# Kernel optimization log

Hardware: AMD Instinct MI355X
Metric: run time of the kernel (lower is better)

Reference implementation:

```python
import jax, jax.numpy as jnp
import numpy as np

HEADS = 8
DIM_HEAD = 64
ROPE_BASE = 10000.0


def _rope_rotate(t):
    """lucidrains-style interleaved RoPE on t: [B, H, N, D]."""
    n, d = t.shape[-2], t.shape[-1]
    inv_freq = 1.0 / (ROPE_BASE ** (jnp.arange(0, d, 2, dtype=jnp.float32) / d))  # [D/2]
    freqs = jnp.arange(n, dtype=jnp.float32)[:, None] * inv_freq[None, :]          # [N, D/2]
    freqs = jnp.repeat(freqs, 2, axis=-1)                                           # [N, D], interleaved
    cos = jnp.cos(freqs).astype(t.dtype)
    sin = jnp.sin(freqs).astype(t.dtype)
    # rotate_half with interleaved pairs: (x1, x2) -> (-x2, x1)
    t2 = t.reshape(t.shape[:-1] + (d // 2, 2))
    rot = jnp.stack([-t2[..., 1], t2[..., 0]], axis=-1).reshape(t.shape)
    return t * cos + rot * sin


def setup_inputs() -> dict:
    key = jax.random.key(0)
    k1, k2, k3, k4 = jax.random.split(key, 4)
    B, N, DIM = 8, 1024, 512
    hidden = HEADS * DIM_HEAD  # 512
    x = jax.random.normal(k1, (B, N, DIM), dtype=jnp.float32)
    pos_bias = jax.random.normal(k2, (HEADS, N, N), dtype=jnp.float32) * 0.1
    w_qkv = jax.random.normal(k3, (DIM, hidden * 3), dtype=jnp.float32) * (DIM ** -0.5)
    w_out = jax.random.normal(k4, (hidden, DIM), dtype=jnp.float32) * (hidden ** -0.5)
    return {"x": x, "pos_bias": pos_bias, "w_qkv": w_qkv, "w_out": w_out}


def reference(x, pos_bias, w_qkv, w_out):
    B, N, _ = x.shape
    qkv = x @ w_qkv                                   # [B, N, 3*H*D]
    q, k, v = jnp.split(qkv, 3, axis=-1)

    def split_heads(t):
        return t.reshape(B, N, HEADS, DIM_HEAD).transpose(0, 2, 1, 3)  # [B, H, N, D]

    q, k, v = map(split_heads, (q, k, v))
    q = q * (DIM_HEAD ** -0.5)
    q = _rope_rotate(q)
    k = _rope_rotate(k)
    sim = jnp.einsum('bhid,bhjd->bhij', q, k) + pos_bias  # pos_bias [H,N,N] broadcasts over B
    attn = jax.nn.softmax(sim, axis=-1)                    # max-subtracted softmax (stable)
    out = jnp.einsum('bhij,bhjd->bhid', attn, v)
    out = out.transpose(0, 2, 1, 3).reshape(B, N, HEADS * DIM_HEAD)
    return out @ w_out
```

## Files before the change

### kernel.cpp

```cpp
#include <hip/hip_runtime.h>

#define DEV __device__ __forceinline__

typedef __attribute__((ext_vector_type(8))) short bf16x8;
typedef __attribute__((ext_vector_type(4))) short bf16x4;
typedef __attribute__((ext_vector_type(4))) float f32x4;
typedef __attribute__((ext_vector_type(4))) unsigned int u32x4;

constexpr int Bb = 8;
constexpr int Nn = 1024;
constexpr int DIMm = 512;
constexpr int Hh = 8;
constexpr int Dh = 64;
constexpr int Mm = Bb * Nn;
constexpr float LN10K = 9.210340371976184f;
constexpr float LOG2E = 1.4426950408889634f;

DEV short f2bf(float f) {
  unsigned int u = __float_as_uint(f);
  u += 0x7fffu + ((u >> 16) & 1u);
  return (short)(u >> 16);
}

DEV unsigned int cvtpk(float lo, float hi) {
  unsigned int r;
  asm("v_cvt_pk_bf16_f32 %0, %1, %2" : "=v"(r) : "v"(lo), "v"(hi));
  return r;
}

DEV bf16x8 comb(bf16x4 lo, bf16x4 hi) {
  bf16x8 r;
  r[0] = lo[0]; r[1] = lo[1]; r[2] = lo[2]; r[3] = lo[3];
  r[4] = hi[0]; r[5] = hi[1]; r[6] = hi[2]; r[7] = hi[3];
  return r;
}

DEV f32x4 mfma16(bf16x8 a, bf16x8 b, f32x4 c) {
  return __builtin_amdgcn_mfma_f32_16x16x32_bf16(a, b, c, 0, 0, 0);
}

DEV void gload16(const void* g, void* l) {
  __builtin_amdgcn_global_load_lds(
      (const __attribute__((address_space(1))) void*)g,
      (__attribute__((address_space(3))) void*)l, 16, 0, 0);
}

__global__ void prep_kernel(const float* __restrict__ x, const float* __restrict__ wq,
                            const float* __restrict__ wo, short* __restrict__ x_bf,
                            short* __restrict__ wqkvT, short* __restrict__ woutT,
                            float2* __restrict__ tab) {
  int stride = gridDim.x * blockDim.x;
  int t = blockIdx.x * blockDim.x + threadIdx.x;
  for (int i = t; i < Mm * DIMm / 4; i += stride) {
    float4 v = ((const float4*)x)[i];
    bf16x4 o;
    o[0] = f2bf(v.x); o[1] = f2bf(v.y); o[2] = f2bf(v.z); o[3] = f2bf(v.w);
    *(bf16x4*)(x_bf + (size_t)i * 4) = o;
  }
  for (int i = t; i < 1536 * 512; i += stride) {
    int n = i >> 9, k = i & 511;
    wqkvT[i] = f2bf(wq[(size_t)k * 1536 + n]);
  }
  for (int i = t; i < 512 * 512; i += stride) {
    int n = i >> 9, k = i & 511;
    woutT[i] = f2bf(wo[(size_t)k * 512 + n]);
  }
  for (int i = t; i < Nn * 32; i += stride) {
    int n = i >> 5, d2 = i & 31;
    float fr = (float)n * __expf(-(float)(2 * d2) * (LN10K / 64.f));
    float sn, cs;
    __sincosf(fr, &sn, &cs);
    tab[i] = make_float2(cs, sn);
  }
}

template <int QKV>
__global__ __launch_bounds__(256) void gemm_k(const short* __restrict__ A,
                                              const short* __restrict__ Bt,
                                              float* __restrict__ outF,
                                              short* __restrict__ qr,
                                              short* __restrict__ kr,
                                              short* __restrict__ vt,
                                              const float2* __restrict__ tab) {
  __shared__ short Al[128][40];
  __shared__ short Bl[128][40];
  const int tid = threadIdx.x;
  const int lane = tid & 63;
  const int wid = tid >> 6;
  const int wm = wid >> 1, wn = wid & 1;
  const int li = lane & 15, g4 = (lane >> 4) << 2;
  const int m0 = blockIdx.x * 128, n0 = blockIdx.y * 128;

  f32x4 zero4 = {0.f, 0.f, 0.f, 0.f};
  f32x4 acc[4][4];
#pragma unroll
  for (int i = 0; i < 4; ++i)
#pragma unroll
    for (int j = 0; j < 4; ++j) acc[i][j] = zero4;

  for (int kt = 0; kt < 512; kt += 32) {
#pragma unroll
    for (int p = 0; p < 2; ++p) {
      int e = (tid + p * 256) * 8;
      int r = e >> 5, c = e & 31;
      *(u32x4*)(&Al[r][c]) = *(const u32x4*)(A + (size_t)(m0 + r) * 512 + kt + c);
      *(u32x4*)(&Bl[r][c]) = *(const u32x4*)(Bt + (size_t)(n0 + r) * 512 + kt + c);
    }
    __syncthreads();
    bf16x8 af[4], bfr[4];
#pragma unroll
    for (int mt = 0; mt < 4; ++mt) {
      int row = wm * 64 + mt * 16 + li;
      af[mt] = comb(*(const bf16x4*)(&Al[row][g4]), *(const bf16x4*)(&Al[row][16 + g4]));
    }
#pragma unroll
    for (int nt = 0; nt < 4; ++nt) {
      int row = wn * 64 + nt * 16 + li;
      bfr[nt] = comb(*(const bf16x4*)(&Bl[row][g4]), *(const bf16x4*)(&Bl[row][16 + g4]));
    }
#pragma unroll
    for (int mt = 0; mt < 4; ++mt)
#pragma unroll
      for (int nt = 0; nt < 4; ++nt)
        acc[mt][nt] = mfma16(af[mt], bfr[nt], acc[mt][nt]);
    __syncthreads();
  }

  if (QKV == 0) {
#pragma unroll
    for (int mt = 0; mt < 4; ++mt) {
      int mb = m0 + wm * 64 + mt * 16 + g4;
#pragma unroll
      for (int nt = 0; nt < 4; ++nt) {
        int c = n0 + wn * 64 + nt * 16 + li;
#pragma unroll
        for (int r = 0; r < 4; ++r) outF[(size_t)(mb + r) * 512 + c] = acc[mt][nt][r];
      }
    }
  } else {
    const int sec = n0 >> 9;
#pragma unroll
    for (int mt = 0; mt < 4; ++mt) {
      int mb = m0 + wm * 64 + mt * 16 + g4;
      int b_ = mb >> 10;
      int nb = mb & 1023;
#pragma unroll
      for (int nt = 0; nt < 4; ++nt) {
        int c = n0 + wn * 64 + nt * 16 + li;
        int cs = c & 511;
        int hh = cs >> 6, d = cs & 63;
        size_t bhoff = (size_t)(b_ * Hh + hh) * 65536;
        if (sec == 2) {
          int dt = d >> 4, liD = d & 15;
          int kkJ = (nb >> 5) & 1;
          int gj = (nb & 15) >> 2;
          int s0 = (nb & 16) >> 2;
          size_t off = bhoff + (size_t)(nb >> 6) * 4096 +
                       (size_t)((dt * 2 + kkJ) * 512) + (size_t)(liD + 16 * gj) * 8 + s0;
          uint2 st;
          st.x = cvtpk(acc[mt][nt][0], acc[mt][nt][1]);
          st.y = cvtpk(acc[mt][nt][2], acc[mt][nt][3]);
          *(uint2*)(vt + off) = st;
        } else {
          int kkD = d >> 5;
          int gd = (d & 15) >> 2;
          int sD = (d & 3) | ((d & 16) >> 2);
          size_t off = bhoff + (size_t)(nb >> 4) * 1024 + (size_t)(kkD * 512) +
                       (size_t)((nb & 15) + 16 * gd) * 8 + sD;
          short* dst = (sec == 0 ? qr : kr) + off;
#pragma unroll
          for (int r = 0; r < 4; ++r) {
            float v0 = acc[mt][nt][r];
            float vp = __shfl_xor(v0, 1, 64);
            float2 cssn = tab[(size_t)(nb + r) * 32 + (d >> 1)];
            float rot = (d & 1) ? vp : -vp;
            float res = v0 * cssn.x + rot * cssn.y;
            if (sec == 0) res *= 0.125f;
            dst[(size_t)r * 8] = f2bf(res);
          }
        }
      }
    }
  }
}

constexpr int KVB = 64;
constexpr int NTT = Nn / KVB;

__global__ __launch_bounds__(256, 4) void attn_k(const short* __restrict__ qf_g,
                                                 const short* __restrict__ kf_g,
                                                 const short* __restrict__ vf_g,
                                                 const float* __restrict__ bias,
                                                 short* __restrict__ ao) {
  __shared__ short Kls[2][4096];
  __shared__ short Vls[2][4096];
  const int tid = threadIdx.x, lane = tid & 63, w = tid >> 6;
  const int li = lane & 15, g4 = (lane >> 4) << 2;
  const int bid = blockIdx.x;
  const int h = bid & 7;
  const int b_ = (bid >> 3) & 7;
  const int it = bid >> 6;
  const int bh = b_ * 8 + h;
  const int i0 = it * 64;
  const int iq = i0 + w * 16 + li;

  const short* qbase = qf_g + (size_t)bh * 65536 + (size_t)(it * 4 + w) * 1024 + lane * 8;
  bf16x8 qf0 = *(const bf16x8*)(qbase);
  bf16x8 qf1 = *(const bf16x8*)(qbase + 512);

  const short* kb = kf_g + (size_t)bh * 65536;
  const short* vb = vf_g + (size_t)bh * 65536;
  const float* br = bias + ((size_t)h * Nn + iq) * Nn + g4;

  float m_run = -1e30f, l_run = 0.f;
  f32x4 zero4 = {0.f, 0.f, 0.f, 0.f};
  f32x4 acc[4];
#pragma unroll
  for (int i = 0; i < 4; ++i) acc[i] = zero4;

#define STAGE_TILE(T, BUF)                                                  \
  do {                                                                      \
    const short* ks_ = kb + (size_t)(T) * 4096;                             \
    const short* vs_ = vb + (size_t)(T) * 4096;                             \
    gload16(ks_ + (size_t)tid * 8, &Kls[BUF][(size_t)(w * 64) * 8]);        \
    gload16(ks_ + (size_t)(256 + tid) * 8,                                  \
            &Kls[BUF][(size_t)(256 + w * 64) * 8]);                         \
    gload16(vs_ + (size_t)tid * 8, &Vls[BUF][(size_t)(w * 64) * 8]);        \
    gload16(vs_ + (size_t)(256 + tid) * 8,                                  \
            &Vls[BUF][(size_t)(256 + w * 64) * 8]);                         \
  } while (0)

  f32x4 bbA[4], bbB[4];

  STAGE_TILE(0, 0);
#pragma unroll
  for (int js = 0; js < 4; ++js) bbA[js] = *(const f32x4*)(br + js * 16);
  asm volatile("s_waitcnt vmcnt(0)" ::: "memory");
  __builtin_amdgcn_s_barrier();

  int cur = 0;
#pragma unroll 1
  for (int t = 0; t < NTT; ++t) {
    if (t + 1 < NTT) {
      STAGE_TILE(t + 1, cur ^ 1);
#pragma unroll
      for (int js = 0; js < 4; ++js)
        bbB[js] = *(const f32x4*)(br + (t + 1) * 64 + js * 16);
    }

    const short* KB = &Kls[cur][0];
    const short* VB = &Vls[cur][0];
    f32x4 s[4];
    __builtin_amdgcn_s_setprio(1);
#pragma unroll
    for (int js = 0; js < 4; ++js) {
      bf16x8 k0 = *(const bf16x8*)(KB + js * 1024 + lane * 8);
      bf16x8 k1 = *(const bf16x8*)(KB + js * 1024 + 512 + lane * 8);
      f32x4 sa = mfma16(k0, qf0, bbA[js]);
      s[js] = mfma16(k1, qf1, sa);
    }
    __builtin_amdgcn_s_setprio(0);

    float mx = fmaxf(fmaxf(fmaxf(s[0][0], s[0][1]), fmaxf(s[0][2], s[0][3])),
                     fmaxf(fmaxf(s[1][0], s[1][1]), fmaxf(s[1][2], s[1][3])));
    float mx2 = fmaxf(fmaxf(fmaxf(s[2][0], s[2][1]), fmaxf(s[2][2], s[2][3])),
                      fmaxf(fmaxf(s[3][0], s[3][1]), fmaxf(s[3][2], s[3][3])));
    mx = fmaxf(mx, mx2);
    mx = fmaxf(mx, __shfl_xor(mx, 16, 64));
    mx = fmaxf(mx, __shfl_xor(mx, 32, 64));

    if (!__all(mx - m_run <= 8.0f)) {
      float mn = fmaxf(m_run, mx);
      float sc = __builtin_amdgcn_exp2f((m_run - mn) * LOG2E);
      l_run *= sc;
      m_run = mn;
      float fs0 = __shfl(sc, g4 + 0, 64), fs1 = __shfl(sc, g4 + 1, 64);
      float fs2 = __shfl(sc, g4 + 2, 64), fs3 = __shfl(sc, g4 + 3, 64);
#pragma unroll
      for (int dt = 0; dt < 4; ++dt) {
        acc[dt][0] *= fs0; acc[dt][1] *= fs1;
        acc[dt][2] *= fs2; acc[dt][3] *= fs3;
      }
    }

    float nm = -m_run * LOG2E;
    float rs = 0.f;
#pragma unroll
    for (int js = 0; js < 4; ++js)
#pragma unroll
      for (int r = 0; r < 4; ++r) {
        float p = __builtin_amdgcn_exp2f(__builtin_fmaf(s[js][r], LOG2E, nm));
        s[js][r] = p;
        rs += p;
      }
    rs += __shfl_xor(rs, 16, 64);
    rs += __shfl_xor(rs, 32, 64);
    l_run += rs;

    bf16x8 pf[2];
#pragma unroll
    for (int kk = 0; kk < 2; ++kk) {
      union { bf16x8 v8; unsigned int d[4]; } u;
      u.d[0] = cvtpk(s[2 * kk][0], s[2 * kk][1]);
      u.d[1] = cvtpk(s[2 * kk][2], s[2 * kk][3]);
      u.d[2] = cvtpk(s[2 * kk + 1][0], s[2 * kk + 1][1]);
      u.d[3] = cvtpk(s[2 * kk + 1][2], s[2 * kk + 1][3]);
      pf[kk] = u.v8;
    }

    __builtin_amdgcn_s_setprio(1);
#pragma unroll
    for (int dt = 0; dt < 4; ++dt) {
      bf16x8 vf0 = *(const bf16x8*)(VB + (dt * 2 + 0) * 512 + lane * 8);
      bf16x8 vf1 = *(const bf16x8*)(VB + (dt * 2 + 1) * 512 + lane * 8);
      f32x4 a = mfma16(pf[0], vf0, acc[dt]);
      acc[dt] = mfma16(pf[1], vf1, a);
    }
    __builtin_amdgcn_s_setprio(0);

    asm volatile("s_waitcnt vmcnt(0)" ::: "memory");
    __builtin_amdgcn_s_barrier();
#pragma unroll
    for (int js = 0; js < 4; ++js) bbA[js] = bbB[js];
    cur ^= 1;
  }
#undef STAGE_TILE

  float rl = 1.f / l_run;
  float fr0 = __shfl(rl, g4 + 0, 64), fr1 = __shfl(rl, g4 + 1, 64);
  float fr2 = __shfl(rl, g4 + 2, 64), fr3 = __shfl(rl, g4 + 3, 64);
#pragma unroll
  for (int dt = 0; dt < 4; ++dt) {
    float fr[4] = {fr0, fr1, fr2, fr3};
#pragma unroll
    for (int r = 0; r < 4; ++r) {
      int i_ = i0 + w * 16 + g4 + r;
      ao[((size_t)(b_ * Nn + i_)) * 512 + h * 64 + dt * 16 + li] =
          f2bf(acc[dt][r] * fr[r]);
    }
  }
}

extern "C" void kernel_launch(void* const* d_in, const int* in_sizes, int n_in,
                              void* d_out, int out_size, void* d_ws, size_t ws_size,
                              hipStream_t stream) {
  const float* x = (const float*)d_in[0];
  const float* pb = (const float*)d_in[1];
  const float* wq = (const float*)d_in[2];
  const float* wo = (const float*)d_in[3];
  float* out = (float*)d_out;

  short* w = (short*)d_ws;
  short* x_bf = w;  w += (size_t)Mm * DIMm;
  short* wqkvT = w; w += 1536 * 512;
  short* woutT = w; w += 512 * 512;
  short* qr = w;    w += (size_t)Mm * DIMm;
  short* kr = w;    w += (size_t)Mm * DIMm;
  short* vt = w;    w += (size_t)Mm * DIMm;
  float2* tab = (float2*)w; w += Nn * 32 * 4;
  short* ao = x_bf;

  prep_kernel<<<1024, 256, 0, stream>>>(x, wq, wo, x_bf, wqkvT, woutT, tab);
  gemm_k<1><<<dim3(64, 12), 256, 0, stream>>>(x_bf, wqkvT, nullptr, qr, kr, vt, tab);
  attn_k<<<1024, 256, 0, stream>>>(qr, kr, vt, pb, ao);
  gemm_k<0><<<dim3(64, 4), 256, 0, stream>>>(ao, woutT, out, nullptr, nullptr, nullptr, tab);
}
```

Before: 117.6 us.

## Enlarge attention query tile to 256 rows with two m-tiles per wave

```diff
diff --git a/kernel.cpp b/kernel.cpp
--- a/kernel.cpp
+++ b/kernel.cpp
@@ -187,7 +187,7 @@
 constexpr int KVB = 64;
 constexpr int NTT = Nn / KVB;
 
-__global__ __launch_bounds__(256, 4) void attn_k(const short* __restrict__ qf_g,
+__global__ __launch_bounds__(512, 2) void attn_k(const short* __restrict__ qf_g,
                                                  const short* __restrict__ kf_g,
                                                  const short* __restrict__ vf_g,
                                                  const float* __restrict__ bias,
@@ -198,43 +198,52 @@
   const int li = lane & 15, g4 = (lane >> 4) << 2;
   const int bid = blockIdx.x;
   const int h = bid & 7;
-  const int b_ = (bid >> 3) & 7;
-  const int it = bid >> 6;
+  const int it = (bid >> 3) & 3;
+  const int b_ = bid >> 5;
   const int bh = b_ * 8 + h;
-  const int i0 = it * 64;
-  const int iq = i0 + w * 16 + li;
-
-  const short* qbase = qf_g + (size_t)bh * 65536 + (size_t)(it * 4 + w) * 1024 + lane * 8;
-  bf16x8 qf0 = *(const bf16x8*)(qbase);
-  bf16x8 qf1 = *(const bf16x8*)(qbase + 512);
+  const int i0 = it * 256;
+  const int iw = i0 + w * 32;
+
+  const short* qb = qf_g + (size_t)bh * 65536 + (size_t)(it * 16 + w * 2) * 1024 +
+                    (size_t)lane * 8;
+  bf16x8 qf[2][2];
+#pragma unroll
+  for (int mt = 0; mt < 2; ++mt)
+#pragma unroll
+    for (int kk = 0; kk < 2; ++kk)
+      qf[mt][kk] = *(const bf16x8*)(qb + mt * 1024 + kk * 512);
 
   const short* kb = kf_g + (size_t)bh * 65536;
   const short* vb = vf_g + (size_t)bh * 65536;
-  const float* br = bias + ((size_t)h * Nn + iq) * Nn + g4;
-
-  float m_run = -1e30f, l_run = 0.f;
+  const float* br0 = bias + ((size_t)h * Nn + iw + li) * Nn + g4;
+  const float* br1 = br0 + (size_t)16 * Nn;
+
+  float m_run[2] = {-1e30f, -1e30f};
+  float l_run[2] = {0.f, 0.f};
   f32x4 zero4 = {0.f, 0.f, 0.f, 0.f};
-  f32x4 acc[4];
-#pragma unroll
-  for (int i = 0; i < 4; ++i) acc[i] = zero4;
-
-#define STAGE_TILE(T, BUF)                                                  \
-  do {                                                                      \
-    const short* ks_ = kb + (size_t)(T) * 4096;                             \
-    const short* vs_ = vb + (size_t)(T) * 4096;                             \
-    gload16(ks_ + (size_t)tid * 8, &Kls[BUF][(size_t)(w * 64) * 8]);        \
-    gload16(ks_ + (size_t)(256 + tid) * 8,                                  \
-            &Kls[BUF][(size_t)(256 + w * 64) * 8]);                         \
-    gload16(vs_ + (size_t)tid * 8, &Vls[BUF][(size_t)(w * 64) * 8]);        \
-    gload16(vs_ + (size_t)(256 + tid) * 8,                                  \
-            &Vls[BUF][(size_t)(256 + w * 64) * 8]);                         \
+  f32x4 acc[4][2];
+#pragma unroll
+  for (int i = 0; i < 4; ++i) {
+    acc[i][0] = zero4;
+    acc[i][1] = zero4;
+  }
+
+#define STAGE_TILE(T, BUF)                                              \
+  do {                                                                  \
+    gload16(kb + (size_t)(T) * 4096 + (size_t)tid * 8,                  \
+            &Kls[BUF][(size_t)(w * 64) * 8]);                           \
+    gload16(vb + (size_t)(T) * 4096 + (size_t)tid * 8,                  \
+            &Vls[BUF][(size_t)(w * 64) * 8]);                           \
   } while (0)
 
-  f32x4 bbA[4], bbB[4];
+  f32x4 bbA[4][2], bbB[4][2];
 
   STAGE_TILE(0, 0);
 #pragma unroll
-  for (int js = 0; js < 4; ++js) bbA[js] = *(const f32x4*)(br + js * 16);
+  for (int js = 0; js < 4; ++js) {
+    bbA[js][0] = *(const f32x4*)(br0 + js * 16);
+    bbA[js][1] = *(const f32x4*)(br1 + js * 16);
+  }
   asm volatile("s_waitcnt vmcnt(0)" ::: "memory");
   __builtin_amdgcn_s_barrier();
 
@@ -244,68 +253,84 @@
     if (t + 1 < NTT) {
       STAGE_TILE(t + 1, cur ^ 1);
 #pragma unroll
-      for (int js = 0; js < 4; ++js)
-        bbB[js] = *(const f32x4*)(br + (t + 1) * 64 + js * 16);
+      for (int js = 0; js < 4; ++js) {
+        bbB[js][0] = *(const f32x4*)(br0 + (t + 1) * 64 + js * 16);
+        bbB[js][1] = *(const f32x4*)(br1 + (t + 1) * 64 + js * 16);
+      }
     }
 
     const short* KB = &Kls[cur][0];
     const short* VB = &Vls[cur][0];
-    f32x4 s[4];
+    f32x4 s[4][2];
     __builtin_amdgcn_s_setprio(1);
 #pragma unroll
     for (int js = 0; js < 4; ++js) {
       bf16x8 k0 = *(const bf16x8*)(KB + js * 1024 + lane * 8);
       bf16x8 k1 = *(const bf16x8*)(KB + js * 1024 + 512 + lane * 8);
-      f32x4 sa = mfma16(k0, qf0, bbA[js]);
-      s[js] = mfma16(k1, qf1, sa);
+#pragma unroll
+      for (int mt = 0; mt < 2; ++mt) {
+        f32x4 sa = mfma16(k0, qf[mt][0], bbA[js][mt]);
+        s[js][mt] = mfma16(k1, qf[mt][1], sa);
+      }
     }
     __builtin_amdgcn_s_setprio(0);
 
-    float mx = fmaxf(fmaxf(fmaxf(s[0][0], s[0][1]), fmaxf(s[0][2], s[0][3])),
-                     fmaxf(fmaxf(s[1][0], s[1][1]), fmaxf(s[1][2], s[1][3])));
-    float mx2 = fmaxf(fmaxf(fmaxf(s[2][0], s[2][1]), fmaxf(s[2][2], s[2][3])),
-                      fmaxf(fmaxf(s[3][0], s[3][1]), fmaxf(s[3][2], s[3][3])));
-    mx = fmaxf(mx, mx2);
-    mx = fmaxf(mx, __shfl_xor(mx, 16, 64));
-    mx = fmaxf(mx, __shfl_xor(mx, 32, 64));
-
-    if (!__all(mx - m_run <= 8.0f)) {
-      float mn = fmaxf(m_run, mx);
-      float sc = __builtin_amdgcn_exp2f((m_run - mn) * LOG2E);
-      l_run *= sc;
-      m_run = mn;
-      float fs0 = __shfl(sc, g4 + 0, 64), fs1 = __shfl(sc, g4 + 1, 64);
-      float fs2 = __shfl(sc, g4 + 2, 64), fs3 = __shfl(sc, g4 + 3, 64);
-#pragma unroll
-      for (int dt = 0; dt < 4; ++dt) {
-        acc[dt][0] *= fs0; acc[dt][1] *= fs1;
-        acc[dt][2] *= fs2; acc[dt][3] *= fs3;
-      }
-    }
-
-    float nm = -m_run * LOG2E;
-    float rs = 0.f;
-#pragma unroll
-    for (int js = 0; js < 4; ++js)
-#pragma unroll
-      for (int r = 0; r < 4; ++r) {
-        float p = __builtin_amdgcn_exp2f(__builtin_fmaf(s[js][r], LOG2E, nm));
-        s[js][r] = p;
-        rs += p;
-      }
-    rs += __shfl_xor(rs, 16, 64);
-    rs += __shfl_xor(rs, 32, 64);
-    l_run += rs;
-
-    bf16x8 pf[2];
-#pragma unroll
-    for (int kk = 0; kk < 2; ++kk) {
-      union { bf16x8 v8; unsigned int d[4]; } u;
-      u.d[0] = cvtpk(s[2 * kk][0], s[2 * kk][1]);
-      u.d[1] = cvtpk(s[2 * kk][2], s[2 * kk][3]);
-      u.d[2] = cvtpk(s[2 * kk + 1][0], s[2 * kk + 1][1]);
-      u.d[3] = cvtpk(s[2 * kk + 1][2], s[2 * kk + 1][3]);
-      pf[kk] = u.v8;
+    float mx[2];
+#pragma unroll
+    for (int mt = 0; mt < 2; ++mt) {
+      float a = fmaxf(fmaxf(fmaxf(s[0][mt][0], s[0][mt][1]), fmaxf(s[0][mt][2], s[0][mt][3])),
+                      fmaxf(fmaxf(s[1][mt][0], s[1][mt][1]), fmaxf(s[1][mt][2], s[1][mt][3])));
+      float b = fmaxf(fmaxf(fmaxf(s[2][mt][0], s[2][mt][1]), fmaxf(s[2][mt][2], s[2][mt][3])),
+                      fmaxf(fmaxf(s[3][mt][0], s[3][mt][1]), fmaxf(s[3][mt][2], s[3][mt][3])));
+      float m = fmaxf(a, b);
+      m = fmaxf(m, __shfl_xor(m, 16, 64));
+      m = fmaxf(m, __shfl_xor(m, 32, 64));
+      mx[mt] = m;
+    }
+
+    bool ok = (mx[0] - m_run[0] <= 8.0f) && (mx[1] - m_run[1] <= 8.0f);
+    if (!__all(ok)) {
+#pragma unroll
+      for (int mt = 0; mt < 2; ++mt) {
+        float mn = fmaxf(m_run[mt], mx[mt]);
+        float sc = __builtin_amdgcn_exp2f((m_run[mt] - mn) * LOG2E);
+        l_run[mt] *= sc;
+        m_run[mt] = mn;
+        float fs0 = __shfl(sc, g4 + 0, 64), fs1 = __shfl(sc, g4 + 1, 64);
+        float fs2 = __shfl(sc, g4 + 2, 64), fs3 = __shfl(sc, g4 + 3, 64);
+#pragma unroll
+        for (int dt = 0; dt < 4; ++dt) {
+          acc[dt][mt][0] *= fs0; acc[dt][mt][1] *= fs1;
+          acc[dt][mt][2] *= fs2; acc[dt][mt][3] *= fs3;
+        }
+      }
+    }
+
+    bf16x8 pf[2][2];
+#pragma unroll
+    for (int mt = 0; mt < 2; ++mt) {
+      float nm = -m_run[mt] * LOG2E;
+      float rs = 0.f;
+#pragma unroll
+      for (int js = 0; js < 4; ++js)
+#pragma unroll
+        for (int r = 0; r < 4; ++r) {
+          float p = __builtin_amdgcn_exp2f(__builtin_fmaf(s[js][mt][r], LOG2E, nm));
+          s[js][mt][r] = p;
+          rs += p;
+        }
+      rs += __shfl_xor(rs, 16, 64);
+      rs += __shfl_xor(rs, 32, 64);
+      l_run[mt] += rs;
+#pragma unroll
+      for (int kk = 0; kk < 2; ++kk) {
+        union { bf16x8 v8; unsigned int d[4]; } u;
+        u.d[0] = cvtpk(s[2 * kk][mt][0], s[2 * kk][mt][1]);
+        u.d[1] = cvtpk(s[2 * kk][mt][2], s[2 * kk][mt][3]);
+        u.d[2] = cvtpk(s[2 * kk + 1][mt][0], s[2 * kk + 1][mt][1]);
+        u.d[3] = cvtpk(s[2 * kk + 1][mt][2], s[2 * kk + 1][mt][3]);
+        pf[kk][mt] = u.v8;
+      }
     }
 
     __builtin_amdgcn_s_setprio(1);
@@ -313,30 +338,39 @@
     for (int dt = 0; dt < 4; ++dt) {
       bf16x8 vf0 = *(const bf16x8*)(VB + (dt * 2 + 0) * 512 + lane * 8);
       bf16x8 vf1 = *(const bf16x8*)(VB + (dt * 2 + 1) * 512 + lane * 8);
-      f32x4 a = mfma16(pf[0], vf0, acc[dt]);
-      acc[dt] = mfma16(pf[1], vf1, a);
+#pragma unroll
+      for (int mt = 0; mt < 2; ++mt) {
+        f32x4 a = mfma16(pf[0][mt], vf0, acc[dt][mt]);
+        acc[dt][mt] = mfma16(pf[1][mt], vf1, a);
+      }
     }
     __builtin_amdgcn_s_setprio(0);
 
     asm volatile("s_waitcnt vmcnt(0)" ::: "memory");
     __builtin_amdgcn_s_barrier();
 #pragma unroll
-    for (int js = 0; js < 4; ++js) bbA[js] = bbB[js];
+    for (int js = 0; js < 4; ++js) {
+      bbA[js][0] = bbB[js][0];
+      bbA[js][1] = bbB[js][1];
+    }
     cur ^= 1;
   }
 #undef STAGE_TILE
 
-  float rl = 1.f / l_run;
-  float fr0 = __shfl(rl, g4 + 0, 64), fr1 = __shfl(rl, g4 + 1, 64);
-  float fr2 = __shfl(rl, g4 + 2, 64), fr3 = __shfl(rl, g4 + 3, 64);
-#pragma unroll
-  for (int dt = 0; dt < 4; ++dt) {
-    float fr[4] = {fr0, fr1, fr2, fr3};
-#pragma unroll
-    for (int r = 0; r < 4; ++r) {
-      int i_ = i0 + w * 16 + g4 + r;
-      ao[((size_t)(b_ * Nn + i_)) * 512 + h * 64 + dt * 16 + li] =
-          f2bf(acc[dt][r] * fr[r]);
+#pragma unroll
+  for (int mt = 0; mt < 2; ++mt) {
+    float rl = 1.f / l_run[mt];
+    float fr0 = __shfl(rl, g4 + 0, 64), fr1 = __shfl(rl, g4 + 1, 64);
+    float fr2 = __shfl(rl, g4 + 2, 64), fr3 = __shfl(rl, g4 + 3, 64);
+#pragma unroll
+    for (int dt = 0; dt < 4; ++dt) {
+      float fr[4] = {fr0, fr1, fr2, fr3};
+#pragma unroll
+      for (int r = 0; r < 4; ++r) {
+        int i_ = iw + mt * 16 + g4 + r;
+        ao[((size_t)(b_ * Nn + i_)) * 512 + h * 64 + dt * 16 + li] =
+            f2bf(acc[dt][mt][r] * fr[r]);
+      }
     }
   }
 }
@@ -362,6 +396,6 @@
 
   prep_kernel<<<1024, 256, 0, stream>>>(x, wq, wo, x_bf, wqkvT, woutT, tab);
   gemm_k<1><<<dim3(64, 12), 256, 0, stream>>>(x_bf, wqkvT, nullptr, qr, kr, vt, tab);
-  attn_k<<<1024, 256, 0, stream>>>(qr, kr, vt, pb, ao);
+  attn_k<<<256, 512, 0, stream>>>(qr, kr, vt, pb, ao);
   gemm_k<0><<<dim3(64, 4), 256, 0, stream>>>(ao, woutT, out, nullptr, nullptr, nullptr, tab);
 }
```

Measured after the change: 126.1 us, median of 3. 1.07x slower.

## Convert position bias to bf16 once and stage it through swizzled LDS

Applied to the files above, without the earlier changes.

```diff
diff --git a/kernel.cpp b/kernel.cpp
--- a/kernel.cpp
+++ b/kernel.cpp
@@ -71,6 +71,18 @@
     float sn, cs;
     __sincosf(fr, &sn, &cs);
     tab[i] = make_float2(cs, sn);
+  }
+}
+
+__global__ void bias_cvt(const float* __restrict__ pb, short* __restrict__ bb) {
+  int stride = gridDim.x * blockDim.x;
+  int t0 = blockIdx.x * blockDim.x + threadIdx.x;
+  for (int i = t0; i < (Hh * Nn * Nn) / 4; i += stride) {
+    float4 v = ((const float4*)pb)[i];
+    uint2 st;
+    st.x = cvtpk(v.x, v.y);
+    st.y = cvtpk(v.z, v.w);
+    *(uint2*)(bb + (size_t)i * 4) = st;
   }
 }
 
@@ -187,13 +199,14 @@
 constexpr int KVB = 64;
 constexpr int NTT = Nn / KVB;
 
-__global__ __launch_bounds__(256, 4) void attn_k(const short* __restrict__ qf_g,
+__global__ __launch_bounds__(256, 3) void attn_k(const short* __restrict__ qf_g,
                                                  const short* __restrict__ kf_g,
                                                  const short* __restrict__ vf_g,
-                                                 const float* __restrict__ bias,
+                                                 const short* __restrict__ bias_bf,
                                                  short* __restrict__ ao) {
   __shared__ short Kls[2][4096];
   __shared__ short Vls[2][4096];
+  __shared__ short Bls[2][4096];
   const int tid = threadIdx.x, lane = tid & 63, w = tid >> 6;
   const int li = lane & 15, g4 = (lane >> 4) << 2;
   const int bid = blockIdx.x;
@@ -202,7 +215,6 @@
   const int it = bid >> 6;
   const int bh = b_ * 8 + h;
   const int i0 = it * 64;
-  const int iq = i0 + w * 16 + li;
 
   const short* qbase = qf_g + (size_t)bh * 65536 + (size_t)(it * 4 + w) * 1024 + lane * 8;
   bf16x8 qf0 = *(const bf16x8*)(qbase);
@@ -210,7 +222,17 @@
 
   const short* kb = kf_g + (size_t)bh * 65536;
   const short* vb = vf_g + (size_t)bh * 65536;
-  const float* br = bias + ((size_t)h * Nn + iq) * Nn + g4;
+
+  const int brow = tid >> 3;
+  const int bchunk = tid & 7;
+  const char* bsrc0 = (const char*)bias_bf + ((size_t)h << 21) +
+                      (size_t)(i0 + brow) * 2048 +
+                      (size_t)((bchunk * 16) ^ ((brow & 7) << 4));
+  const char* bsrc1 = bsrc0 + (size_t)32 * 2048;
+
+  const int q8 = (lane >> 4) << 3;
+  const int bswz = (li & 7) << 4;
+  const int brd_row = (w * 16 + li) * 128;
 
   float m_run = -1e30f, l_run = 0.f;
   f32x4 zero4 = {0.f, 0.f, 0.f, 0.f};
@@ -228,35 +250,36 @@
     gload16(vs_ + (size_t)tid * 8, &Vls[BUF][(size_t)(w * 64) * 8]);        \
     gload16(vs_ + (size_t)(256 + tid) * 8,                                  \
             &Vls[BUF][(size_t)(256 + w * 64) * 8]);                         \
+    gload16(bsrc0 + (size_t)(T) * 128, &Bls[BUF][(size_t)(w * 64) * 8]);    \
+    gload16(bsrc1 + (size_t)(T) * 128,                                      \
+            &Bls[BUF][(size_t)(256 + w * 64) * 8]);                         \
   } while (0)
 
-  f32x4 bbA[4], bbB[4];
-
   STAGE_TILE(0, 0);
-#pragma unroll
-  for (int js = 0; js < 4; ++js) bbA[js] = *(const f32x4*)(br + js * 16);
   asm volatile("s_waitcnt vmcnt(0)" ::: "memory");
   __builtin_amdgcn_s_barrier();
 
   int cur = 0;
 #pragma unroll 1
   for (int t = 0; t < NTT; ++t) {
-    if (t + 1 < NTT) {
-      STAGE_TILE(t + 1, cur ^ 1);
-#pragma unroll
-      for (int js = 0; js < 4; ++js)
-        bbB[js] = *(const f32x4*)(br + (t + 1) * 64 + js * 16);
-    }
+    if (t + 1 < NTT) STAGE_TILE(t + 1, cur ^ 1);
 
     const short* KB = &Kls[cur][0];
     const short* VB = &Vls[cur][0];
+    const char* BP = (const char*)&Bls[cur][0] + brd_row;
     f32x4 s[4];
     __builtin_amdgcn_s_setprio(1);
 #pragma unroll
     for (int js = 0; js < 4; ++js) {
+      uint2 bd = *(const uint2*)(BP + ((js * 32 + q8) ^ bswz));
+      f32x4 bb;
+      bb[0] = __uint_as_float(bd.x << 16);
+      bb[1] = __uint_as_float(bd.x & 0xffff0000u);
+      bb[2] = __uint_as_float(bd.y << 16);
+      bb[3] = __uint_as_float(bd.y & 0xffff0000u);
       bf16x8 k0 = *(const bf16x8*)(KB + js * 1024 + lane * 8);
       bf16x8 k1 = *(const bf16x8*)(KB + js * 1024 + 512 + lane * 8);
-      f32x4 sa = mfma16(k0, qf0, bbA[js]);
+      f32x4 sa = mfma16(k0, qf0, bb);
       s[js] = mfma16(k1, qf1, sa);
     }
     __builtin_amdgcn_s_setprio(0);
@@ -320,8 +343,6 @@
 
     asm volatile("s_waitcnt vmcnt(0)" ::: "memory");
     __builtin_amdgcn_s_barrier();
-#pragma unroll
-    for (int js = 0; js < 4; ++js) bbA[js] = bbB[js];
     cur ^= 1;
   }
 #undef STAGE_TILE
@@ -358,10 +379,12 @@
   short* kr = w;    w += (size_t)Mm * DIMm;
   short* vt = w;    w += (size_t)Mm * DIMm;
   float2* tab = (float2*)w; w += Nn * 32 * 4;
+  short* bias_bf = w; w += (size_t)Hh * Nn * Nn;
   short* ao = x_bf;
 
   prep_kernel<<<1024, 256, 0, stream>>>(x, wq, wo, x_bf, wqkvT, woutT, tab);
   gemm_k<1><<<dim3(64, 12), 256, 0, stream>>>(x_bf, wqkvT, nullptr, qr, kr, vt, tab);
-  attn_k<<<1024, 256, 0, stream>>>(qr, kr, vt, pb, ao);
+  bias_cvt<<<2048, 256, 0, stream>>>(pb, bias_bf);
+  attn_k<<<1024, 256, 0, stream>>>(qr, kr, vt, bias_bf, ao);
   gemm_k<0><<<dim3(64, 4), 256, 0, stream>>>(ao, woutT, out, nullptr, nullptr, nullptr, tab);
 }
```

New measurement: 123.9 us. 5.3% more time.
